# Kernel tuning notes

Hardware: AMD Instinct MI355X
Metric: run time of the kernel (lower is better)

The kernel has to match this reference:

```python
import jax, jax.numpy as jnp
import numpy as np

N_EMBD = 384
N_HEAD = 6
HEAD_SIZE = N_EMBD // N_HEAD  # 64
BLOCK = 64
EPS = 1e-5


def _layernorm(x, g, b):
    mu = jnp.mean(x, axis=-1, keepdims=True)
    var = jnp.mean(jnp.square(x - mu), axis=-1, keepdims=True)
    return (x - mu) * jax.lax.rsqrt(var + EPS) * g + b


def setup_inputs() -> dict:
    key = jax.random.key(0)
    ks = jax.random.split(key, 12)
    s = 0.02
    return {
        "x": jax.random.normal(ks[0], (1024, BLOCK, N_EMBD), dtype=jnp.float32),
        "ln1_g": jnp.ones((N_EMBD,), jnp.float32),
        "ln1_b": jnp.zeros((N_EMBD,), jnp.float32),
        "Wq": jax.random.normal(ks[1], (N_HEAD, N_EMBD, HEAD_SIZE), jnp.float32) * s,
        "Wk": jax.random.normal(ks[2], (N_HEAD, N_EMBD, HEAD_SIZE), jnp.float32) * s,
        "Wv": jax.random.normal(ks[3], (N_HEAD, N_EMBD, HEAD_SIZE), jnp.float32) * s,
        "Wo": jax.random.normal(ks[4], (N_EMBD, N_EMBD), jnp.float32) * s,
        "bo": jnp.zeros((N_EMBD,), jnp.float32),
        "ln2_g": jnp.ones((N_EMBD,), jnp.float32),
        "ln2_b": jnp.zeros((N_EMBD,), jnp.float32),
        "W1": jax.random.normal(ks[5], (N_EMBD, 4 * N_EMBD), jnp.float32) * s,
        "b1": jnp.zeros((4 * N_EMBD,), jnp.float32),
        "W2": jax.random.normal(ks[6], (4 * N_EMBD, N_EMBD), jnp.float32) * s,
        "b2": jnp.zeros((N_EMBD,), jnp.float32),
    }


def reference(x, ln1_g, ln1_b, Wq, Wk, Wv, Wo, bo, ln2_g, ln2_b, W1, b1, W2, b2):
    B, T, C = x.shape
    # --- multi-head causal self-attention on ln1(x) ---
    xn = _layernorm(x, ln1_g, ln1_b)
    q = jnp.einsum('btc,hcd->bhtd', xn, Wq)
    k = jnp.einsum('btc,hcd->bhtd', xn, Wk)
    v = jnp.einsum('btc,hcd->bhtd', xn, Wv)
    scale = HEAD_SIZE ** -0.5
    att = jnp.einsum('bhtd,bhsd->bhts', q, k) * scale
    causal = jnp.tril(jnp.ones((T, T), bool))
    att = jnp.where(causal, att, -jnp.inf)
    att = jax.nn.softmax(att, axis=-1)  # dropout is identity at eval
    out = jnp.einsum('bhts,bhsd->bhtd', att, v)
    out = out.transpose(0, 2, 1, 3).reshape(B, T, C)  # concat heads
    x = x + out @ Wo + bo
    # --- feed-forward on ln2(x) ---
    xn2 = _layernorm(x, ln2_g, ln2_b)
    h = jax.nn.relu(xn2 @ W1 + b1)
    x = x + h @ W2 + b2
    return x
```

## Files before the change

kernel.cpp:

```cpp
#include <hip/hip_runtime.h>

#define TT 64
#define CC 384
#define NH 6
#define HID 1536
#define LDX 392
#define LDH 72

typedef __bf16 bf16x8 __attribute__((ext_vector_type(8)));
typedef float f32x4 __attribute__((ext_vector_type(4)));
typedef unsigned short us8 __attribute__((ext_vector_type(8)));

#define MFMA(a, b, c) __builtin_amdgcn_mfma_f32_16x16x32_bf16(a, b, c, 0, 0, 0)
#define WAITVM(N) asm volatile("s_waitcnt vmcnt(" #N ")" ::: "memory")

static __device__ __forceinline__ unsigned short f2bf(float f) {
  unsigned u = __builtin_bit_cast(unsigned, f);
  u += 0x7FFFu + ((u >> 16) & 1u);
  return (unsigned short)(u >> 16);
}
static __device__ __forceinline__ float bf2f(unsigned short h) {
  unsigned u = ((unsigned)h) << 16;
  return __builtin_bit_cast(float, u);
}
static __device__ __forceinline__ bf16x8 ld8(const unsigned short* p) {
  return __builtin_bit_cast(bf16x8, *reinterpret_cast<const us8*>(p));
}
static __device__ __forceinline__ void glds16(const unsigned short* g, unsigned short* l) {
  __builtin_amdgcn_global_load_lds(
      (const __attribute__((address_space(1))) void*)g,
      (__attribute__((address_space(3))) void*)l, 16, 0, 0);
}

__global__ void prep_w(const float* __restrict__ Wq, const float* __restrict__ Wk,
                       const float* __restrict__ Wv, const float* __restrict__ Wo,
                       const float* __restrict__ W1, const float* __restrict__ W2,
                       unsigned short* __restrict__ ws) {
  const int T0 = 1152 * 384;
  const int T1 = T0 + 384 * 384;
  const int T2 = T1 + 1536 * 384;
  const int T3 = T2 + 384 * 1536;
  for (int i = blockIdx.x * blockDim.x + threadIdx.x; i < T3; i += gridDim.x * blockDim.x) {
    float v;
    if (i < T0) {
      int n = i / 384, k = i % 384;
      int hh = n / 192, j = n % 192;
      const float* W = (j < 64) ? Wq : (j < 128) ? Wk : Wv;
      int d = (j < 64) ? j : (j < 128) ? j - 64 : j - 128;
      v = W[((size_t)hh * 384 + k) * 64 + d];
    } else if (i < T1) {
      int i2 = i - T0; int n = i2 / 384, k = i2 % 384;
      v = Wo[(size_t)k * 384 + n];
    } else if (i < T2) {
      int i2 = i - T1; int n = i2 / 384, k = i2 % 384;
      v = W1[(size_t)k * 1536 + n];
    } else {
      int i2 = i - T2; int n = i2 / 1536, k = i2 % 1536;
      v = W2[(size_t)k * 384 + n];
    }
    ws[i] = f2bf(v);
  }
}

__global__ __launch_bounds__(256, 2)
void attn_fwd(const float* __restrict__ x,
              const float* __restrict__ ln1g, const float* __restrict__ ln1b,
              const float* __restrict__ bo,
              const unsigned short* __restrict__ Wqkv,
              const unsigned short* __restrict__ WoT,
              float* __restrict__ x2) {
  __shared__ unsigned short sXN[TT * LDX];
  __shared__ unsigned short sHEAD[3 * TT * LDH];
  unsigned short* sQ = sHEAD;
  unsigned short* sK = sHEAD + TT * LDH;
  unsigned short* sV = sHEAD + 2 * TT * LDH;

  const int b = blockIdx.x;
  const int tid = threadIdx.x;
  const int wv = tid >> 6;
  const int ln = tid & 63;
  const int l16 = ln & 15;
  const int lg = ln >> 4;
  const float* xb = x + (size_t)b * TT * CC;
  const f32x4 Z4 = {0.f, 0.f, 0.f, 0.f};

#pragma unroll 1
  for (int r = wv * 16; r < wv * 16 + 16; ++r) {
    float v[6], s = 0.f, sq = 0.f;
#pragma unroll
    for (int j = 0; j < 6; ++j) { v[j] = xb[r * CC + ln + 64 * j]; s += v[j]; sq += v[j] * v[j]; }
#pragma unroll
    for (int off = 32; off; off >>= 1) { s += __shfl_xor(s, off); sq += __shfl_xor(sq, off); }
    float mu = s * (1.f / CC);
    float rs = rsqrtf(sq * (1.f / CC) - mu * mu + 1e-5f);
#pragma unroll
    for (int j = 0; j < 6; ++j) {
      int c = ln + 64 * j;
      sXN[r * LDX + c] = f2bf((v[j] - mu) * rs * ln1g[c] + ln1b[c]);
    }
  }
  __syncthreads();

  f32x4 pacc[4][6];
#pragma unroll
  for (int m = 0; m < 4; ++m)
#pragma unroll
    for (int c = 0; c < 6; ++c) pacc[m][c] = Z4;

  const unsigned short* prow[6];
#pragma unroll
  for (int c = 0; c < 6; ++c)
    prow[c] = WoT + (size_t)(wv * 96 + c * 16 + l16) * CC + 8 * lg;

#pragma unroll 1
  for (int h = 0; h < NH; ++h) {
    const unsigned short* wrow[3];
#pragma unroll
    for (int c = 0; c < 3; ++c)
      wrow[c] = Wqkv + (size_t)(h * 192 + wv * 48 + c * 16 + l16) * CC + 8 * lg;

    f32x4 qacc[4][3];
#pragma unroll
    for (int m = 0; m < 4; ++m)
#pragma unroll
      for (int c = 0; c < 3; ++c) qacc[m][c] = Z4;

    bf16x8 bpre[2][3];
#pragma unroll
    for (int c = 0; c < 3; ++c) bpre[0][c] = ld8(wrow[c] + 0);
#pragma unroll
    for (int c = 0; c < 3; ++c) bpre[1][c] = ld8(wrow[c] + 32);
#pragma unroll
    for (int kk = 0; kk < CC; kk += 32) {
      const int slot = (kk >> 5) & 1;
      bf16x8 bcur[3];
#pragma unroll
      for (int c = 0; c < 3; ++c) bcur[c] = bpre[slot][c];
      if (kk + 64 < CC) {
#pragma unroll
        for (int c = 0; c < 3; ++c) bpre[slot][c] = ld8(wrow[c] + kk + 64);
      }
      bf16x8 a[4];
#pragma unroll
      for (int m = 0; m < 4; ++m)
        a[m] = ld8(&sXN[(m * 16 + l16) * LDX + kk + 8 * lg]);
      __builtin_amdgcn_s_setprio(1);
#pragma unroll
      for (int c = 0; c < 3; ++c)
#pragma unroll
        for (int m = 0; m < 4; ++m) qacc[m][c] = MFMA(a[m], bcur[c], qacc[m][c]);
      __builtin_amdgcn_s_setprio(0);
    }
    __syncthreads();
#pragma unroll
    for (int m = 0; m < 4; ++m)
#pragma unroll
      for (int c = 0; c < 3; ++c) {
        int n = wv * 48 + c * 16 + l16;
#pragma unroll
        for (int rg = 0; rg < 4; ++rg) {
          int t = m * 16 + lg * 4 + rg;
          unsigned short bv = f2bf(qacc[m][c][rg]);
          if (n < 64) sQ[t * LDH + n] = bv;
          else if (n < 128) sK[t * LDH + (n - 64)] = bv;
          else sV[(n - 128) * LDH + t] = bv;
        }
      }
    __syncthreads();

    f32x4 sacc[4];
#pragma unroll
    for (int c = 0; c < 4; ++c) sacc[c] = Z4;
#pragma unroll
    for (int kk = 0; kk < 64; kk += 32) {
      bf16x8 a = ld8(&sQ[(wv * 16 + l16) * LDH + kk + 8 * lg]);
#pragma unroll
      for (int c = 0; c < 4; ++c) {
        bf16x8 bb = ld8(&sK[(c * 16 + l16) * LDH + kk + 8 * lg]);
        sacc[c] = MFMA(a, bb, sacc[c]);
      }
    }
#pragma unroll
    for (int rg = 0; rg < 4; ++rg) {
      int row = wv * 16 + lg * 4 + rg;
      float e[4], mx = -1e30f;
#pragma unroll
      for (int c = 0; c < 4; ++c) {
        int col = c * 16 + l16;
        float vv = sacc[c][rg] * 0.125f;
        e[c] = (col <= row) ? vv : -1e30f;
        mx = fmaxf(mx, e[c]);
      }
#pragma unroll
      for (int off = 8; off; off >>= 1) mx = fmaxf(mx, __shfl_xor(mx, off));
      float sum = 0.f;
#pragma unroll
      for (int c = 0; c < 4; ++c) {
        int col = c * 16 + l16;
        e[c] = (col <= row) ? __expf(e[c] - mx) : 0.f;
        sum += e[c];
      }
#pragma unroll
      for (int off = 8; off; off >>= 1) sum += __shfl_xor(sum, off);
      float inv = 1.f / sum;
#pragma unroll
      for (int c = 0; c < 4; ++c)
        sQ[row * LDH + c * 16 + l16] = f2bf(e[c] * inv);
    }

    bf16x8 pb[2][6];
#pragma unroll
    for (int s2 = 0; s2 < 2; ++s2)
#pragma unroll
      for (int c = 0; c < 6; ++c)
        pb[s2][c] = ld8(prow[c] + h * 64 + 32 * s2);

    f32x4 oacc[4];
#pragma unroll
    for (int c = 0; c < 4; ++c) oacc[c] = Z4;
#pragma unroll
    for (int kk = 0; kk < 64; kk += 32) {
      bf16x8 a = ld8(&sQ[(wv * 16 + l16) * LDH + kk + 8 * lg]);
#pragma unroll
      for (int c = 0; c < 4; ++c) {
        bf16x8 bb = ld8(&sV[(c * 16 + l16) * LDH + kk + 8 * lg]);
        oacc[c] = MFMA(a, bb, oacc[c]);
      }
    }
    __syncthreads();
#pragma unroll
    for (int c = 0; c < 4; ++c)
#pragma unroll
      for (int rg = 0; rg < 4; ++rg) {
        int t = wv * 16 + lg * 4 + rg;
        sK[t * LDH + c * 16 + l16] = f2bf(oacc[c][rg]);
      }
    __syncthreads();

    __builtin_amdgcn_s_setprio(1);
#pragma unroll
    for (int kk = 0; kk < 64; kk += 32) {
      const int slot = kk >> 5;
      bf16x8 a[4];
#pragma unroll
      for (int m = 0; m < 4; ++m)
        a[m] = ld8(&sK[(m * 16 + l16) * LDH + kk + 8 * lg]);
#pragma unroll
      for (int c = 0; c < 6; ++c)
#pragma unroll
        for (int m = 0; m < 4; ++m) pacc[m][c] = MFMA(a[m], pb[slot][c], pacc[m][c]);
    }
    __builtin_amdgcn_s_setprio(0);
  }

  float* xo = x2 + (size_t)b * TT * CC;
#pragma unroll
  for (int m = 0; m < 4; ++m)
#pragma unroll
    for (int c = 0; c < 6; ++c) {
      int n = wv * 96 + c * 16 + l16;
      float bov = bo[n];
#pragma unroll
      for (int rg = 0; rg < 4; ++rg) {
        int t = m * 16 + lg * 4 + rg;
        xo[t * CC + n] = xb[t * CC + n] + pacc[m][c][rg] + bov;
      }
    }
}

__global__ __launch_bounds__(512, 2)
void mlp_fwd(const float* __restrict__ ln2g, const float* __restrict__ ln2b,
             const float* __restrict__ b1, const float* __restrict__ b2,
             const unsigned short* __restrict__ W1T,
             const unsigned short* __restrict__ W2T,
             float* xo) {
  __shared__ unsigned short sXN[24576];
  __shared__ unsigned short sH[8192];
  __shared__ unsigned short sW[8192];

  const int b = blockIdx.x;
  const int tid = threadIdx.x;
  const int wv = tid >> 6;
  const int ln = tid & 63;
  const int l16 = ln & 15;
  const int lg = ln >> 4;
  float* xb = xo + (size_t)b * TT * CC;
  const f32x4 Z4 = {0.f, 0.f, 0.f, 0.f};
  unsigned short* myW = sW + wv * 1024;
  const int rx = (l16 ^ lg) << 3;

#pragma unroll 1
  for (int r = wv * 8; r < wv * 8 + 8; ++r) {
    float v[6], s = 0.f, sq = 0.f;
#pragma unroll
    for (int j = 0; j < 6; ++j) { v[j] = xb[r * CC + ln + 64 * j]; s += v[j]; sq += v[j] * v[j]; }
#pragma unroll
    for (int off = 32; off; off >>= 1) { s += __shfl_xor(s, off); sq += __shfl_xor(sq, off); }
    float mu = s * (1.f / CC);
    float rs = rsqrtf(sq * (1.f / CC) - mu * mu + 1e-5f);
    int m = r >> 4, row16 = r & 15;
#pragma unroll
    for (int j = 0; j < 6; ++j) {
      int c = ln + 64 * j;
      int sl = c >> 5, ks = (c >> 3) & 3, off = c & 7;
      sXN[(((m * 12 + sl) * 4 + ks) * 16 + (row16 ^ ks)) * 8 + off] =
          f2bf((v[j] - mu) * rs * ln2g[c] + ln2b[c]);
    }
  }
  __syncthreads();

#define G1S(CH, SL)                                                             \
  glds16(W1T + (size_t)((CH) * 128 + wv * 16 + (ln >> 2)) * CC + (SL) * 32 +    \
             (ln & 3) * 8,                                                      \
         myW + ((SL) & 1) * 512)

#define G1C(SL) do {                                                            \
    bf16x8 a_[4];                                                               \
    _Pragma("unroll")                                                           \
    for (int m = 0; m < 4; ++m)                                                 \
      a_[m] = ld8(&sXN[((m * 48 + (SL) * 4 + lg) << 7) + rx]);                  \
    bf16x8 bb_ = ld8(&myW[((SL) & 1) * 512 + l16 * 32 + lg * 8]);               \
    __builtin_amdgcn_s_setprio(1);                                              \
    _Pragma("unroll")                                                           \
    for (int m = 0; m < 4; ++m) hacc[m] = MFMA(a_[m], bb_, hacc[m]);            \
    __builtin_amdgcn_s_setprio(0);                                              \
  } while (0)

  f32x4 macc[4][3];
#pragma unroll
  for (int m = 0; m < 4; ++m)
#pragma unroll
    for (int c = 0; c < 3; ++c) macc[m][c] = Z4;

  G1S(0, 0); G1S(0, 1);

#pragma unroll 1
  for (int ch = 0; ch < 12; ++ch) {
    f32x4 hacc[4];
#pragma unroll
    for (int m = 0; m < 4; ++m) hacc[m] = Z4;

    WAITVM(1); G1C(0);  G1S(ch, 2);
    WAITVM(1); G1C(1);  G1S(ch, 3);
    WAITVM(1); G1C(2);  G1S(ch, 4);
    WAITVM(1); G1C(3);  G1S(ch, 5);
    WAITVM(1); G1C(4);  G1S(ch, 6);
    WAITVM(1); G1C(5);  G1S(ch, 7);
    WAITVM(1); G1C(6);  G1S(ch, 8);
    WAITVM(1); G1C(7);  G1S(ch, 9);
    WAITVM(1); G1C(8);  G1S(ch, 10);
    WAITVM(1); G1C(9);  G1S(ch, 11);
    WAITVM(1); G1C(10);
    WAITVM(0); G1C(11);

    float b1v = b1[ch * 128 + wv * 16 + l16];
    const unsigned short* w2p = W2T + (size_t)(wv * 48 + l16) * HID + ch * 128 + 8 * lg;
    bf16x8 c2[3];
#pragma unroll
    for (int c = 0; c < 3; ++c) c2[c] = ld8(w2p + (size_t)(c * 16) * HID);

    __syncthreads();

    {
      int nl = wv * 16 + l16;
      int slh = nl >> 5, ks = (nl >> 3) & 3, off = nl & 7;
#pragma unroll
      for (int m = 0; m < 4; ++m)
#pragma unroll
        for (int rg = 0; rg < 4; ++rg) {
          int row16 = lg * 4 + rg;
          sH[(((m * 4 + slh) * 4 + ks) * 16 + (row16 ^ ks)) * 8 + off] =
              f2bf(fmaxf(hacc[m][rg] + b1v, 0.f));
        }
    }
    __syncthreads();

#pragma unroll
    for (int sl = 0; sl < 4; ++sl) {
      bf16x8 a2[4];
#pragma unroll
      for (int m = 0; m < 4; ++m)
        a2[m] = ld8(&sH[((m * 16 + sl * 4 + lg) << 7) + rx]);
      bf16x8 nxt[3];
      if (sl < 3) {
#pragma unroll
        for (int c = 0; c < 3; ++c) nxt[c] = ld8(w2p + (size_t)(c * 16) * HID + (sl + 1) * 32);
      }
      if (sl == 2 && ch < 11) {
        G1S(ch + 1, 0); G1S(ch + 1, 1);
      }
      __builtin_amdgcn_s_setprio(1);
#pragma unroll
      for (int c = 0; c < 3; ++c)
#pragma unroll
        for (int m = 0; m < 4; ++m) macc[m][c] = MFMA(a2[m], c2[c], macc[m][c]);
      __builtin_amdgcn_s_setprio(0);
      if (sl < 3) {
#pragma unroll
        for (int c = 0; c < 3; ++c) c2[c] = nxt[c];
      }
    }
  }

#pragma unroll
  for (int m = 0; m < 4; ++m)
#pragma unroll
    for (int c = 0; c < 3; ++c) {
      int n = wv * 48 + c * 16 + l16;
      float b2v = b2[n];
#pragma unroll
      for (int rg = 0; rg < 4; ++rg) {
        int t = m * 16 + lg * 4 + rg;
        size_t idx = (size_t)t * CC + n;
        float x2v = xb[idx];
        xb[idx] = x2v + macc[m][c][rg] + b2v;
      }
    }
#undef G1S
#undef G1C
}

extern "C" void kernel_launch(void* const* d_in, const int* in_sizes, int n_in,
                              void* d_out, int out_size, void* d_ws, size_t ws_size,
                              hipStream_t stream) {
  const float* x    = (const float*)d_in[0];
  const float* ln1g = (const float*)d_in[1];
  const float* ln1b = (const float*)d_in[2];
  const float* Wq   = (const float*)d_in[3];
  const float* Wk   = (const float*)d_in[4];
  const float* Wv   = (const float*)d_in[5];
  const float* Wo   = (const float*)d_in[6];
  const float* bo   = (const float*)d_in[7];
  const float* ln2g = (const float*)d_in[8];
  const float* ln2b = (const float*)d_in[9];
  const float* W1   = (const float*)d_in[10];
  const float* b1   = (const float*)d_in[11];
  const float* W2   = (const float*)d_in[12];
  const float* b2   = (const float*)d_in[13];
  unsigned short* ws = (unsigned short*)d_ws;

  const size_t need = (size_t)(1152 * 384 + 384 * 384 + 1536 * 384 + 384 * 1536) * 2;
  if (ws_size < need) return;

  hipLaunchKernelGGL(prep_w, dim3(1024), dim3(256), 0, stream, Wq, Wk, Wv, Wo, W1, W2, ws);

  const unsigned short* Wqkv = ws;
  const unsigned short* WoT  = ws + 1152 * 384;
  const unsigned short* W1T  = WoT + 384 * 384;
  const unsigned short* W2T  = W1T + 1536 * 384;
  int nblk = in_sizes[0] / (TT * CC);

  hipLaunchKernelGGL(attn_fwd, dim3(nblk), dim3(256), 0, stream,
                     x, ln1g, ln1b, bo, Wqkv, WoT, (float*)d_out);
  hipLaunchKernelGGL(mlp_fwd, dim3(nblk), dim3(512), 0, stream,
                     ln2g, ln2b, b1, b2, W1T, W2T, (float*)d_out);
}
```

Measured before the change: 508.9 us.

## Halve MLP block to four waves with wider per-wave tiles

New measurement: 440.8 us. 1.15x faster.

```diff
diff --git a/kernel.cpp b/kernel.cpp
--- a/kernel.cpp
+++ b/kernel.cpp
@@ -268,7 +268,7 @@
     }
 }
 
-__global__ __launch_bounds__(512, 2)
+__global__ __launch_bounds__(256, 2)
 void mlp_fwd(const float* __restrict__ ln2g, const float* __restrict__ ln2b,
              const float* __restrict__ b1, const float* __restrict__ b2,
              const unsigned short* __restrict__ W1T,
@@ -286,11 +286,11 @@
   const int lg = ln >> 4;
   float* xb = xo + (size_t)b * TT * CC;
   const f32x4 Z4 = {0.f, 0.f, 0.f, 0.f};
-  unsigned short* myW = sW + wv * 1024;
+  unsigned short* myW = sW + wv * 2048;
   const int rx = (l16 ^ lg) << 3;
 
 #pragma unroll 1
-  for (int r = wv * 8; r < wv * 8 + 8; ++r) {
+  for (int r = wv * 16; r < wv * 16 + 16; ++r) {
     float v[6], s = 0.f, sq = 0.f;
 #pragma unroll
     for (int j = 0; j < 6; ++j) { v[j] = xb[r * CC + ln + 64 * j]; s += v[j]; sq += v[j] * v[j]; }
@@ -309,70 +309,84 @@
   }
   __syncthreads();
 
-#define G1S(CH, SL)                                                             \
-  glds16(W1T + (size_t)((CH) * 128 + wv * 16 + (ln >> 2)) * CC + (SL) * 32 +    \
-             (ln & 3) * 8,                                                      \
-         myW + ((SL) & 1) * 512)
+#define G1S(CH, SL) do {                                                        \
+    _Pragma("unroll")                                                           \
+    for (int j = 0; j < 2; ++j)                                                 \
+      glds16(W1T + (size_t)((CH) * 128 + wv * 32 + j * 16 + (ln >> 2)) * CC +   \
+                 (SL) * 32 + (ln & 3) * 8,                                      \
+             myW + ((SL) & 1) * 1024 + j * 512);                                \
+  } while (0)
 
 #define G1C(SL) do {                                                            \
     bf16x8 a_[4];                                                               \
     _Pragma("unroll")                                                           \
     for (int m = 0; m < 4; ++m)                                                 \
       a_[m] = ld8(&sXN[((m * 48 + (SL) * 4 + lg) << 7) + rx]);                  \
-    bf16x8 bb_ = ld8(&myW[((SL) & 1) * 512 + l16 * 32 + lg * 8]);               \
     __builtin_amdgcn_s_setprio(1);                                              \
     _Pragma("unroll")                                                           \
-    for (int m = 0; m < 4; ++m) hacc[m] = MFMA(a_[m], bb_, hacc[m]);            \
+    for (int c = 0; c < 2; ++c) {                                               \
+      bf16x8 bb_ = ld8(&myW[((SL) & 1) * 1024 + c * 512 + l16 * 32 + lg * 8]);  \
+      _Pragma("unroll")                                                         \
+      for (int m = 0; m < 4; ++m) hacc[m][c] = MFMA(a_[m], bb_, hacc[m][c]);    \
+    }                                                                           \
     __builtin_amdgcn_s_setprio(0);                                              \
   } while (0)
 
-  f32x4 macc[4][3];
+  f32x4 macc[4][6];
 #pragma unroll
   for (int m = 0; m < 4; ++m)
 #pragma unroll
-    for (int c = 0; c < 3; ++c) macc[m][c] = Z4;
-
-  G1S(0, 0); G1S(0, 1);
+    for (int c = 0; c < 6; ++c) macc[m][c] = Z4;
+
+  const unsigned short* w2base = W2T + (size_t)(wv * 96 + l16) * HID + 8 * lg;
+
+  G1S(0, 0);
 
 #pragma unroll 1
   for (int ch = 0; ch < 12; ++ch) {
-    f32x4 hacc[4];
-#pragma unroll
-    for (int m = 0; m < 4; ++m) hacc[m] = Z4;
-
-    WAITVM(1); G1C(0);  G1S(ch, 2);
-    WAITVM(1); G1C(1);  G1S(ch, 3);
-    WAITVM(1); G1C(2);  G1S(ch, 4);
-    WAITVM(1); G1C(3);  G1S(ch, 5);
-    WAITVM(1); G1C(4);  G1S(ch, 6);
-    WAITVM(1); G1C(5);  G1S(ch, 7);
-    WAITVM(1); G1C(6);  G1S(ch, 8);
-    WAITVM(1); G1C(7);  G1S(ch, 9);
-    WAITVM(1); G1C(8);  G1S(ch, 10);
-    WAITVM(1); G1C(9);  G1S(ch, 11);
-    WAITVM(1); G1C(10);
-    WAITVM(0); G1C(11);
-
-    float b1v = b1[ch * 128 + wv * 16 + l16];
-    const unsigned short* w2p = W2T + (size_t)(wv * 48 + l16) * HID + ch * 128 + 8 * lg;
-    bf16x8 c2[3];
-#pragma unroll
-    for (int c = 0; c < 3; ++c) c2[c] = ld8(w2p + (size_t)(c * 16) * HID);
-
-    __syncthreads();
-
-    {
-      int nl = wv * 16 + l16;
-      int slh = nl >> 5, ks = (nl >> 3) & 3, off = nl & 7;
-#pragma unroll
-      for (int m = 0; m < 4; ++m)
+    f32x4 hacc[4][2];
+#pragma unroll
+    for (int m = 0; m < 4; ++m)
+#pragma unroll
+      for (int c = 0; c < 2; ++c) hacc[m][c] = Z4;
+
+    G1S(ch, 1);  WAITVM(2); G1C(0);
+    G1S(ch, 2);  WAITVM(2); G1C(1);
+    G1S(ch, 3);  WAITVM(2); G1C(2);
+    G1S(ch, 4);  WAITVM(2); G1C(3);
+    G1S(ch, 5);  WAITVM(2); G1C(4);
+    G1S(ch, 6);  WAITVM(2); G1C(5);
+    G1S(ch, 7);  WAITVM(2); G1C(6);
+    G1S(ch, 8);  WAITVM(2); G1C(7);
+    G1S(ch, 9);  WAITVM(2); G1C(8);
+    G1S(ch, 10); WAITVM(2); G1C(9);
+    G1S(ch, 11); WAITVM(2); G1C(10);
+    WAITVM(0);   G1C(11);
+
+    float b1c[2];
+#pragma unroll
+    for (int c = 0; c < 2; ++c) b1c[c] = b1[ch * 128 + wv * 32 + c * 16 + l16];
+    const unsigned short* w2p = w2base + ch * 128;
+    bf16x8 c2[6];
+#pragma unroll
+    for (int c = 0; c < 6; ++c) c2[c] = ld8(w2p + (size_t)(c * 16) * HID);
+    if (ch < 11) G1S(ch + 1, 0);
+
+    __syncthreads();
+
+#pragma unroll
+    for (int m = 0; m < 4; ++m)
+#pragma unroll
+      for (int c = 0; c < 2; ++c) {
+        int nl = wv * 32 + c * 16 + l16;
+        int slh = nl >> 5, ks = (nl >> 3) & 3, off = nl & 7;
 #pragma unroll
         for (int rg = 0; rg < 4; ++rg) {
           int row16 = lg * 4 + rg;
           sH[(((m * 4 + slh) * 4 + ks) * 16 + (row16 ^ ks)) * 8 + off] =
-              f2bf(fmaxf(hacc[m][rg] + b1v, 0.f));
+              f2bf(fmaxf(hacc[m][c][rg] + b1c[c], 0.f));
         }
-    }
+      }
     __syncthreads();
 
 #pragma unroll
@@ -381,23 +395,20 @@
 #pragma unroll
       for (int m = 0; m < 4; ++m)
         a2[m] = ld8(&sH[((m * 16 + sl * 4 + lg) << 7) + rx]);
-      bf16x8 nxt[3];
+      bf16x8 nxt[6];
       if (sl < 3) {
 #pragma unroll
-        for (int c = 0; c < 3; ++c) nxt[c] = ld8(w2p + (size_t)(c * 16) * HID + (sl + 1) * 32);
-      }
-      if (sl == 2 && ch < 11) {
-        G1S(ch + 1, 0); G1S(ch + 1, 1);
+        for (int c = 0; c < 6; ++c) nxt[c] = ld8(w2p + (size_t)(c * 16) * HID + (sl + 1) * 32);
       }
       __builtin_amdgcn_s_setprio(1);
 #pragma unroll
-      for (int c = 0; c < 3; ++c)
+      for (int c = 0; c < 6; ++c)
 #pragma unroll
         for (int m = 0; m < 4; ++m) macc[m][c] = MFMA(a2[m], c2[c], macc[m][c]);
       __builtin_amdgcn_s_setprio(0);
       if (sl < 3) {
 #pragma unroll
-        for (int c = 0; c < 3; ++c) c2[c] = nxt[c];
+        for (int c = 0; c < 6; ++c) c2[c] = nxt[c];
       }
     }
   }
@@ -405,8 +416,8 @@
 #pragma unroll
   for (int m = 0; m < 4; ++m)
 #pragma unroll
-    for (int c = 0; c < 3; ++c) {
-      int n = wv * 48 + c * 16 + l16;
+    for (int c = 0; c < 6; ++c) {
+      int n = wv * 96 + c * 16 + l16;
       float b2v = b2[n];
 #pragma unroll
       for (int rg = 0; rg < 4; ++rg) {
@@ -452,6 +463,6 @@
 
   hipLaunchKernelGGL(attn_fwd, dim3(nblk), dim3(256), 0, stream,
                      x, ln1g, ln1b, bo, Wqkv, WoT, (float*)d_out);
-  hipLaunchKernelGGL(mlp_fwd, dim3(nblk), dim3(512), 0, stream,
+  hipLaunchKernelGGL(mlp_fwd, dim3(nblk), dim3(256), 0, stream,
                      ln2g, ln2b, b1, b2, W1T, W2T, (float*)d_out);
 }
```
